# Performance work log

Measured on AMD Instinct MI355X. Metric: run time of the kernel, lower is better.

Reference implementation:

```python
import jax, jax.numpy as jnp
import numpy as np

KERNEL_SIZE = 2
DILATION = 2


def aconv(x, A, shift):
    # x: [n, c, v, l], A: [v, w]; temporal roll + zero-mask first `shift` steps,
    # then node diffusion x . A over the node axis.
    xr = jnp.roll(x, shift, axis=3)
    if shift > 0:
        xr = xr.at[..., :shift].set(0.0)
    return jnp.einsum('ncvl,vw->ncwl', xr, A)


def setup_inputs() -> dict:
    key = jax.random.key(0)
    ks = jax.random.split(key, 7)
    N, C, V, L, E, CO = 32, 64, 500, 64, 10, 64
    return {
        'x': jax.random.normal(ks[0], (N, C, V, L), dtype=jnp.float32),
        'nodevec1': jax.random.normal(ks[1], (V, E), dtype=jnp.float32),
        'nodevec2': jax.random.normal(ks[2], (E, V), dtype=jnp.float32),
        'et_w': jax.random.normal(ks[3], (E, E), dtype=jnp.float32),
        'et_b': jax.random.normal(ks[4], (E,), dtype=jnp.float32),
        'mlp_w': jax.random.normal(ks[5], (CO, (1 + KERNEL_SIZE) * C), dtype=jnp.float32) * 0.05,
        'mlp_b': jax.random.normal(ks[6], (CO,), dtype=jnp.float32),
    }


def reference(x, nodevec1, nodevec2, et_w, et_b, mlp_w, mlp_b):
    out = [x]
    x2 = x
    shift = 0
    # hop 0: adaptive adjacency from node embeddings
    adp = jax.nn.softmax(jax.nn.relu(nodevec1 @ nodevec2), axis=1)
    x1 = aconv(x2, adp, shift)
    out.append(x1)
    shift = DILATION
    x2 = x1
    for i in range(KERNEL_SIZE - 1):
        # emb_trans: affine update of both node embeddings
        nodevec1 = nodevec1 @ et_w + et_b
        nodevec2 = (nodevec2.T @ et_w + et_b).T
        adp = jax.nn.softmax(jax.nn.relu(nodevec1 @ nodevec2), axis=1)
        x1 = aconv(x2, adp, shift)
        out.append(x1)
        shift = shift + DILATION
        x2 = x1
    h = jnp.concatenate(out, axis=1)  # [n, (1+K)*c, v, l]
    # 1x1 conv == channel matmul; dropout is identity at inference
    h = jnp.einsum('ncvl,oc->novl', h, mlp_w) + mlp_b[None, :, None, None]
    return h
```

## Files before the change

### kernel.cpp

```cpp
#include <hip/hip_runtime.h>
#include <hip/hip_bf16.h>

#define NB 32
#define CC 64
#define VV 500
#define LL 64
#define EE 10
#define CO 64
#define DIL 2
#define VP 512
#define SL (VV * LL)

typedef unsigned short u16;
typedef unsigned int   u32;
typedef __attribute__((ext_vector_type(8))) short bf16x8;
typedef __attribute__((ext_vector_type(4))) float f32x4;

__device__ __forceinline__ float bf2f(u16 u) {
    union { u32 i; float f; } c; c.i = ((u32)u) << 16; return c.f;
}
__device__ __forceinline__ u16 f2bf(float f) {
    union { float f; u32 i; } c; c.f = f;
    u32 x = c.i;
    u32 r = (x + 0x7fffu + ((x >> 16) & 1u)) >> 16;
    return (u16)r;
}

__global__ void emb_kernel(const float* __restrict__ nv1, const float* __restrict__ nv2,
                           const float* __restrict__ et_w, const float* __restrict__ et_b,
                           const float* __restrict__ mlp_w,
                           float* __restrict__ nv1t, float* __restrict__ nv2t,
                           u16* __restrict__ wb) {
    int idx = blockIdx.x * blockDim.x + threadIdx.x;
    if (idx < VV * EE) {
        int v = idx / EE, e = idx - v * EE;
        float s = et_b[e];
        #pragma unroll
        for (int f = 0; f < EE; f++) s += nv1[v * EE + f] * et_w[f * EE + e];
        nv1t[idx] = s;
    } else if (idx < 2 * VV * EE) {
        int k = idx - VV * EE;
        int e = k / VV, v = k - e * VV;
        float s = et_b[e];
        #pragma unroll
        for (int f = 0; f < EE; f++) s += nv2[f * VV + v] * et_w[f * EE + e];
        nv2t[k] = s;
    } else if (idx < 2 * VV * EE + CO * 3 * CC) {
        int k = idx - 2 * VV * EE;
        wb[k] = f2bf(mlp_w[k]);
    }
}

__global__ __launch_bounds__(64) void adj2_kernel(const float* __restrict__ nv1,
                                                  const float* __restrict__ nv2,
                                                  const float* __restrict__ nv1t,
                                                  const float* __restrict__ nv2t,
                                                  u16* __restrict__ Atb0,
                                                  u16* __restrict__ Atb1) {
    const int which = blockIdx.x >> 9;
    const int v = blockIdx.x & (VP - 1);
    const float* p1 = which ? nv1t : nv1;
    const float* p2 = which ? nv2t : nv2;
    u16* Atb = which ? Atb1 : Atb0;
    const int lane = threadIdx.x;
    if (v >= VV) {
        #pragma unroll
        for (int j = 0; j < 8; j++) Atb[(size_t)(lane + 64 * j) * VP + v] = 0;
        return;
    }
    float e1[EE];
    #pragma unroll
    for (int e = 0; e < EE; e++) e1[e] = p1[v * EE + e];

    float r[8];
    float m = -1e30f;
    #pragma unroll
    for (int j = 0; j < 8; j++) {
        int w = lane + 64 * j;
        if (w < VV) {
            float s = 0.f;
            #pragma unroll
            for (int e = 0; e < EE; e++) s += e1[e] * p2[e * VV + w];
            r[j] = fmaxf(s, 0.f);
            m = fmaxf(m, r[j]);
        } else {
            r[j] = -1e30f;
        }
    }
    #pragma unroll
    for (int off = 32; off > 0; off >>= 1) m = fmaxf(m, __shfl_xor(m, off));

    float p[8];
    float sum = 0.f;
    #pragma unroll
    for (int j = 0; j < 8; j++) {
        int w = lane + 64 * j;
        if (w < VV) { p[j] = expf(r[j] - m); sum += p[j]; }
    }
    #pragma unroll
    for (int off = 32; off > 0; off >>= 1) sum += __shfl_xor(sum, off);
    float inv = 1.f / sum;
    #pragma unroll
    for (int j = 0; j < 8; j++) {
        int w = lane + 64 * j;
        Atb[(size_t)w * VP + v] = (w < VV) ? f2bf(p[j] * inv) : (u16)0;
    }
}

__global__ __launch_bounds__(512, 2) void hops_fused(const float* __restrict__ x,
                                                     const u16* __restrict__ Atb0,
                                                     const u16* __restrict__ Atb1,
                                                     u16* __restrict__ x1g,
                                                     u16* __restrict__ x2g) {
    __shared__ u16 Xt[2][LL * VP];
    const int bid = blockIdx.x;
    const int tid = threadIdx.x;
    const int lane = tid & 63;
    const int wv = tid >> 6;
    const int wr = wv * 64;
    const size_t base0 = (size_t)(2 * bid) * (VV * LL);
    const size_t base1 = base0 + (VV * LL);

    {
        const int lquad = lane & 15;
        const int vsub = lane >> 4;
        const int l0 = 4 * lquad;
        #pragma unroll
        for (int pl = 0; pl < 2; ++pl) {
            char* ldsb = (char*)Xt[pl];
            const float* xp = x + (pl ? base1 : base0);
            #pragma unroll
            for (int i = 0; i < 8; ++i) {
                const int vp = wv * 32 + i * 4 + vsub;
                const int v0 = 2 * vp;
                u32 pk0, pk1, pk2, pk3;
                if (v0 < VV) {
                    const float* xa = xp + v0 * LL + l0;
                    float4 fa = *(const float4*)xa;
                    float4 fb = *(const float4*)(xa + LL);
                    pk0 = (u32)f2bf(fa.x) | ((u32)f2bf(fb.x) << 16);
                    pk1 = (u32)f2bf(fa.y) | ((u32)f2bf(fb.y) << 16);
                    pk2 = (u32)f2bf(fa.z) | ((u32)f2bf(fb.z) << 16);
                    pk3 = (u32)f2bf(fa.w) | ((u32)f2bf(fb.w) << 16);
                } else {
                    pk0 = pk1 = pk2 = pk3 = 0;
                }
                const int vb = 4 * vp;
                int l = l0;
                *(u32*)(ldsb + l * (VP * 2) + (vb ^ ((l & 7) << 4))) = pk0; l++;
                *(u32*)(ldsb + l * (VP * 2) + (vb ^ ((l & 7) << 4))) = pk1; l++;
                *(u32*)(ldsb + l * (VP * 2) + (vb ^ ((l & 7) << 4))) = pk2; l++;
                *(u32*)(ldsb + l * (VP * 2) + (vb ^ ((l & 7) << 4))) = pk3;
            }
        }
    }
    __syncthreads();

    const int r15 = lane & 15;
    const int kg = lane >> 4;
    const char* lds0 = (const char*)Xt[0];
    const char* lds1 = (const char*)Xt[1];
    int lrow[4], lswz[4];
    #pragma unroll
    for (int ct = 0; ct < 4; ct++) {
        const int l = ct * 16 + r15;
        lrow[ct] = l * (VP * 2);
        lswz[ct] = (l & 7) << 4;
    }
    const u16* arow0[4];
    const u16* arow1[4];
    #pragma unroll
    for (int rt = 0; rt < 4; rt++) {
        const size_t ro = (size_t)(wr + rt * 16 + r15) * VP + kg * 8;
        arow0[rt] = Atb0 + ro;
        arow1[rt] = Atb1 + ro;
    }

    f32x4 acc0[4][4], acc1[4][4];
    #pragma unroll
    for (int rt = 0; rt < 4; rt++)
        #pragma unroll
        for (int ct = 0; ct < 4; ct++) {
            acc0[rt][ct] = (f32x4){0.f, 0.f, 0.f, 0.f};
            acc1[rt][ct] = (f32x4){0.f, 0.f, 0.f, 0.f};
        }

    #pragma unroll
    for (int kb = 0; kb < VP; kb += 32) {
        bf16x8 a[4], b0[4], b1[4];
        #pragma unroll
        for (int rt = 0; rt < 4; rt++)
            a[rt] = *(const bf16x8*)(arow0[rt] + kb);
        #pragma unroll
        for (int ct = 0; ct < 4; ct++) {
            const int ko = (kb * 2 + kg * 16) ^ lswz[ct];
            b0[ct] = *(const bf16x8*)(lds0 + lrow[ct] + ko);
            b1[ct] = *(const bf16x8*)(lds1 + lrow[ct] + ko);
        }
        __builtin_amdgcn_s_setprio(1);
        #pragma unroll
        for (int rt = 0; rt < 4; rt++)
            #pragma unroll
            for (int ct = 0; ct < 4; ct++) {
                acc0[rt][ct] = __builtin_amdgcn_mfma_f32_16x16x32_bf16(a[rt], b0[ct], acc0[rt][ct], 0, 0, 0);
                acc1[rt][ct] = __builtin_amdgcn_mfma_f32_16x16x32_bf16(a[rt], b1[ct], acc1[rt][ct], 0, 0, 0);
            }
        __builtin_amdgcn_s_setprio(0);
    }

    #pragma unroll
    for (int pl = 0; pl < 2; ++pl) {
        u16* xo = x1g + (pl ? base1 : base0);
        #pragma unroll
        for (int rt = 0; rt < 4; rt++) {
            #pragma unroll
            for (int ct = 0; ct < 4; ct++) {
                const int col = ct * 16 + r15;
                const int wbase = wr + rt * 16 + kg * 4;
                f32x4 c = pl ? acc1[rt][ct] : acc0[rt][ct];
                #pragma unroll
                for (int r = 0; r < 4; r++) {
                    int w = wbase + r;
                    if (w < VV) xo[w * LL + col] = f2bf(c[r]);
                }
            }
        }
    }
    __syncthreads();

    {
        #pragma unroll
        for (int pl = 0; pl < 2; ++pl) {
            char* ldsw = (char*)Xt[pl];
            {
                const int l = tid >> 8;
                const int j = tid & 255;
                *(u32*)(ldsw + l * (VP * 2) + 4 * j) = 0;
            }
            #pragma unroll
            for (int rt = 0; rt < 4; rt++) {
                const int wb2 = (wr + rt * 16 + kg * 4) * 2;
                #pragma unroll
                for (int ct = 0; ct < 4; ct++) {
                    const int col = ct * 16 + r15;
                    const int ln = col + DIL;
                    if (ln < LL) {
                        f32x4 c = pl ? acc1[rt][ct] : acc0[rt][ct];
                        u32 plo = (u32)f2bf(c[0]) | ((u32)f2bf(c[1]) << 16);
                        u32 phi = (u32)f2bf(c[2]) | ((u32)f2bf(c[3]) << 16);
                        const int swz = (ln & 7) << 4;
                        char* p = ldsw + ln * (VP * 2);
                        *(u32*)(p + (wb2 ^ swz)) = plo;
                        *(u32*)(p + ((wb2 + 4) ^ swz)) = phi;
                    }
                }
            }
        }
    }
    __syncthreads();

    #pragma unroll
    for (int rt = 0; rt < 4; rt++)
        #pragma unroll
        for (int ct = 0; ct < 4; ct++) {
            acc0[rt][ct] = (f32x4){0.f, 0.f, 0.f, 0.f};
            acc1[rt][ct] = (f32x4){0.f, 0.f, 0.f, 0.f};
        }

    #pragma unroll
    for (int kb = 0; kb < VP; kb += 32) {
        bf16x8 a[4], b0[4], b1[4];
        #pragma unroll
        for (int rt = 0; rt < 4; rt++)
            a[rt] = *(const bf16x8*)(arow1[rt] + kb);
        #pragma unroll
        for (int ct = 0; ct < 4; ct++) {
            const int ko = (kb * 2 + kg * 16) ^ lswz[ct];
            b0[ct] = *(const bf16x8*)(lds0 + lrow[ct] + ko);
            b1[ct] = *(const bf16x8*)(lds1 + lrow[ct] + ko);
        }
        __builtin_amdgcn_s_setprio(1);
        #pragma unroll
        for (int rt = 0; rt < 4; rt++)
            #pragma unroll
            for (int ct = 0; ct < 4; ct++) {
                acc0[rt][ct] = __builtin_amdgcn_mfma_f32_16x16x32_bf16(a[rt], b0[ct], acc0[rt][ct], 0, 0, 0);
                acc1[rt][ct] = __builtin_amdgcn_mfma_f32_16x16x32_bf16(a[rt], b1[ct], acc1[rt][ct], 0, 0, 0);
            }
        __builtin_amdgcn_s_setprio(0);
    }

    #pragma unroll
    for (int pl = 0; pl < 2; ++pl) {
        u16* xo = x2g + (pl ? base1 : base0);
        #pragma unroll
        for (int rt = 0; rt < 4; rt++) {
            #pragma unroll
            for (int ct = 0; ct < 4; ct++) {
                const int col = ct * 16 + r15;
                const int wbase = wr + rt * 16 + kg * 4;
                f32x4 c = pl ? acc1[rt][ct] : acc0[rt][ct];
                #pragma unroll
                for (int r = 0; r < 4; r++) {
                    int w = wbase + r;
                    if (w < VV) xo[w * LL + col] = f2bf(c[r]);
                }
            }
        }
    }
}

__global__ __launch_bounds__(256, 3) void mlp_mfma(const float* __restrict__ x,
                                                   const u16* __restrict__ x1,
                                                   const u16* __restrict__ x2,
                                                   const u16* __restrict__ wb,
                                                   const float* __restrict__ b,
                                                   float* __restrict__ out) {
    __shared__ u16 Ht[128 * 192];
    const int bid = blockIdx.x;
    const int n = bid / (SL / 128);
    const int st = bid - n * (SL / 128);
    const int s0 = st * 128;
    const int tid = threadIdx.x;

    const int lane = tid & 63;
    const int wv = tid >> 6;
    const int obase = (wv & 1) * 32;
    const int sbase = (wv >> 1) * 64;
    const int r15 = lane & 15;
    const int kg = lane >> 4;

    bf16x8 afrag[2][6];
    #pragma unroll
    for (int rt = 0; rt < 2; rt++)
        #pragma unroll
        for (int ks = 0; ks < 6; ks++)
            afrag[rt][ks] = *(const bf16x8*)(wb + (obase + rt * 16 + r15) * (3 * CC) + ks * 32 + kg * 8);

    {
        char* ldsb = (char*)Ht;
        const int squad = tid >> 3;
        const int pgroup = tid & 7;
        const int sq0 = 4 * squad;
        #pragma unroll
        for (int i = 0; i < 12; ++i) {
            const int P = i * 8 + pgroup;
            const int c = 2 * P;
            u32 pk0, pk1, pk2, pk3;
            if (i < 4) {
                const float* fsrc = x + ((size_t)n * CC + c) * SL + s0 + sq0;
                float4 va = *(const float4*)fsrc;
                float4 vb = *(const float4*)(fsrc + SL);
                pk0 = (u32)f2bf(va.x) | ((u32)f2bf(vb.x) << 16);
                pk1 = (u32)f2bf(va.y) | ((u32)f2bf(vb.y) << 16);
                pk2 = (u32)f2bf(va.z) | ((u32)f2bf(vb.z) << 16);
                pk3 = (u32)f2bf(va.w) | ((u32)f2bf(vb.w) << 16);
            } else {
                const u16* bsrc = (i < 8)
                    ? x1 + ((size_t)n * CC + (c - CC)) * SL + s0 + sq0
                    : x2 + ((size_t)n * CC + (c - 2 * CC)) * SL + s0 + sq0;
                uint2 va = *(const uint2*)bsrc;
                uint2 vb = *(const uint2*)(bsrc + SL);
                pk0 = (va.x & 0xffffu) | (vb.x << 16);
                pk1 = (va.x >> 16) | (vb.x & 0xffff0000u);
                pk2 = (va.y & 0xffffu) | (vb.y << 16);
                pk3 = (va.y >> 16) | (vb.y & 0xffff0000u);
            }
            int s = sq0;
            *(u32*)(ldsb + s * 384 + ((4 * P) ^ ((s & 7) << 4))) = pk0; s++;
            *(u32*)(ldsb + s * 384 + ((4 * P) ^ ((s & 7) << 4))) = pk1; s++;
            *(u32*)(ldsb + s * 384 + ((4 * P) ^ ((s & 7) << 4))) = pk2; s++;
            *(u32*)(ldsb + s * 384 + ((4 * P) ^ ((s & 7) << 4))) = pk3;
        }
    }
    __syncthreads();

    f32x4 acc[2][4];
    #pragma unroll
    for (int rt = 0; rt < 2; rt++)
        #pragma unroll
        for (int ct = 0; ct < 4; ct++)
            acc[rt][ct] = (f32x4){0.f, 0.f, 0.f, 0.f};

    const char* ldsb = (const char*)Ht;
    #pragma unroll
    for (int ks = 0; ks < 6; ks++) {
        bf16x8 bfr[4];
        #pragma unroll
        for (int ct = 0; ct < 4; ct++) {
            const int s = sbase + ct * 16 + r15;
            bfr[ct] = *(const bf16x8*)(ldsb + s * 384 + ((ks * 64 + kg * 16) ^ ((s & 7) << 4)));
        }
        #pragma unroll
        for (int rt = 0; rt < 2; rt++)
            #pragma unroll
            for (int ct = 0; ct < 4; ct++)
                acc[rt][ct] = __builtin_amdgcn_mfma_f32_16x16x32_bf16(afrag[rt][ks], bfr[ct], acc[rt][ct], 0, 0, 0);
    }

    #pragma unroll
    for (int rt = 0; rt < 2; rt++) {
        #pragma unroll
        for (int r = 0; r < 4; r++) {
            const int o = obase + rt * 16 + kg * 4 + r;
            const float bias = b[o];
            float* orow = out + ((size_t)n * CO + o) * SL + s0 + sbase;
            #pragma unroll
            for (int ct = 0; ct < 4; ct++)
                orow[ct * 16 + r15] = acc[rt][ct][r] + bias;
        }
    }
}

extern "C" void kernel_launch(void* const* d_in, const int* in_sizes, int n_in,
                              void* d_out, int out_size, void* d_ws, size_t ws_size,
                              hipStream_t stream) {
    const float* x     = (const float*)d_in[0];
    const float* nv1   = (const float*)d_in[1];
    const float* nv2   = (const float*)d_in[2];
    const float* et_w  = (const float*)d_in[3];
    const float* et_b  = (const float*)d_in[4];
    const float* mlp_w = (const float*)d_in[5];
    const float* mlp_b = (const float*)d_in[6];
    float* out = (float*)d_out;

    char* wsb = (char*)d_ws;
    size_t off = 0;
    auto alloc = [&](size_t bytes) {
        size_t o = off;
        off += (bytes + 255) & ~(size_t)255;
        return o;
    };
    u16*   Atb0 = (u16*)(wsb + alloc((size_t)VP * VP * 2));
    u16*   Atb1 = (u16*)(wsb + alloc((size_t)VP * VP * 2));
    float* nv1t = (float*)(wsb + alloc((size_t)VV * EE * 4));
    float* nv2t = (float*)(wsb + alloc((size_t)EE * VV * 4));
    u16*   wb   = (u16*)(wsb + alloc((size_t)CO * 3 * CC * 2));
    u16*   x1   = (u16*)(wsb + alloc((size_t)NB * CC * VV * LL * 2));
    u16*   x2   = (u16*)(wsb + alloc((size_t)NB * CC * VV * LL * 2));
    (void)in_sizes; (void)n_in; (void)out_size; (void)ws_size;

    const int embN = 2 * VV * EE + CO * 3 * CC;
    emb_kernel<<<(embN + 255) / 256, 256, 0, stream>>>(nv1, nv2, et_w, et_b, mlp_w, nv1t, nv2t, wb);
    adj2_kernel<<<2 * VP, 64, 0, stream>>>(nv1, nv2, nv1t, nv2t, Atb0, Atb1);
    hops_fused<<<NB * CC / 2, 512, 0, stream>>>(x, Atb0, Atb1, x1, x2);
    mlp_mfma<<<NB * (SL / 128), 256, 0, stream>>>(x, x1, x2, wb, mlp_b, out);
}
```

Measured before the change: 445.7 us.

## Pipeline plane-1 staging behind plane-0 MFMA and process planes sequentially

The hop kernel now processes the two batch planes one after another with a single accumulator set instead of two interleaved sets. The global load and bf16 conversion of the second plane's input into LDS is software-pipelined inside the first plane's MFMA loop, hiding that load latency behind compute. Write-backs and the shifted LDS rewrites are interleaved between per-plane GEMMs. Halving the accumulators reduces register pressure, at the cost of less MFMA independence per k-step and extra barriers.

```diff
diff --git a/kernel.cpp b/kernel.cpp
--- a/kernel.cpp
+++ b/kernel.cpp
@@ -121,45 +121,12 @@
     const size_t base0 = (size_t)(2 * bid) * (VV * LL);
     const size_t base1 = base0 + (VV * LL);
 
-    {
-        const int lquad = lane & 15;
-        const int vsub = lane >> 4;
-        const int l0 = 4 * lquad;
-        #pragma unroll
-        for (int pl = 0; pl < 2; ++pl) {
-            char* ldsb = (char*)Xt[pl];
-            const float* xp = x + (pl ? base1 : base0);
-            #pragma unroll
-            for (int i = 0; i < 8; ++i) {
-                const int vp = wv * 32 + i * 4 + vsub;
-                const int v0 = 2 * vp;
-                u32 pk0, pk1, pk2, pk3;
-                if (v0 < VV) {
-                    const float* xa = xp + v0 * LL + l0;
-                    float4 fa = *(const float4*)xa;
-                    float4 fb = *(const float4*)(xa + LL);
-                    pk0 = (u32)f2bf(fa.x) | ((u32)f2bf(fb.x) << 16);
-                    pk1 = (u32)f2bf(fa.y) | ((u32)f2bf(fb.y) << 16);
-                    pk2 = (u32)f2bf(fa.z) | ((u32)f2bf(fb.z) << 16);
-                    pk3 = (u32)f2bf(fa.w) | ((u32)f2bf(fb.w) << 16);
-                } else {
-                    pk0 = pk1 = pk2 = pk3 = 0;
-                }
-                const int vb = 4 * vp;
-                int l = l0;
-                *(u32*)(ldsb + l * (VP * 2) + (vb ^ ((l & 7) << 4))) = pk0; l++;
-                *(u32*)(ldsb + l * (VP * 2) + (vb ^ ((l & 7) << 4))) = pk1; l++;
-                *(u32*)(ldsb + l * (VP * 2) + (vb ^ ((l & 7) << 4))) = pk2; l++;
-                *(u32*)(ldsb + l * (VP * 2) + (vb ^ ((l & 7) << 4))) = pk3;
-            }
-        }
-    }
-    __syncthreads();
-
+    const int lquad = lane & 15;
+    const int vsub = lane >> 4;
+    const int l0 = 4 * lquad;
     const int r15 = lane & 15;
     const int kg = lane >> 4;
-    const char* lds0 = (const char*)Xt[0];
-    const char* lds1 = (const char*)Xt[1];
+
     int lrow[4], lswz[4];
     #pragma unroll
     for (int ct = 0; ct < 4; ct++) {
@@ -176,48 +143,39 @@
         arow1[rt] = Atb1 + ro;
     }
 
-    f32x4 acc0[4][4], acc1[4][4];
-    #pragma unroll
-    for (int rt = 0; rt < 4; rt++)
-        #pragma unroll
-        for (int ct = 0; ct < 4; ct++) {
-            acc0[rt][ct] = (f32x4){0.f, 0.f, 0.f, 0.f};
-            acc1[rt][ct] = (f32x4){0.f, 0.f, 0.f, 0.f};
-        }
-
-    #pragma unroll
-    for (int kb = 0; kb < VP; kb += 32) {
-        bf16x8 a[4], b0[4], b1[4];
+    f32x4 acc[4][4];
+
+    auto zacc = [&]() {
         #pragma unroll
         for (int rt = 0; rt < 4; rt++)
-            a[rt] = *(const bf16x8*)(arow0[rt] + kb);
-        #pragma unroll
-        for (int ct = 0; ct < 4; ct++) {
-            const int ko = (kb * 2 + kg * 16) ^ lswz[ct];
-            b0[ct] = *(const bf16x8*)(lds0 + lrow[ct] + ko);
-            b1[ct] = *(const bf16x8*)(lds1 + lrow[ct] + ko);
-        }
+            #pragma unroll
+            for (int ct = 0; ct < 4; ct++)
+                acc[rt][ct] = (f32x4){0.f, 0.f, 0.f, 0.f};
+    };
+    auto kstep = [&](const u16* const arow[4], const char* ldsX, int s) {
+        bf16x8 a[4], b[4];
+        #pragma unroll
+        for (int rt = 0; rt < 4; rt++)
+            a[rt] = *(const bf16x8*)(arow[rt] + s * 32);
+        #pragma unroll
+        for (int ct = 0; ct < 4; ct++)
+            b[ct] = *(const bf16x8*)(ldsX + lrow[ct] + ((s * 64 + kg * 16) ^ lswz[ct]));
         __builtin_amdgcn_s_setprio(1);
         #pragma unroll
         for (int rt = 0; rt < 4; rt++)
             #pragma unroll
-            for (int ct = 0; ct < 4; ct++) {
-                acc0[rt][ct] = __builtin_amdgcn_mfma_f32_16x16x32_bf16(a[rt], b0[ct], acc0[rt][ct], 0, 0, 0);
-                acc1[rt][ct] = __builtin_amdgcn_mfma_f32_16x16x32_bf16(a[rt], b1[ct], acc1[rt][ct], 0, 0, 0);
-            }
+            for (int ct = 0; ct < 4; ct++)
+                acc[rt][ct] = __builtin_amdgcn_mfma_f32_16x16x32_bf16(a[rt], b[ct], acc[rt][ct], 0, 0, 0);
         __builtin_amdgcn_s_setprio(0);
-    }
-
-    #pragma unroll
-    for (int pl = 0; pl < 2; ++pl) {
-        u16* xo = x1g + (pl ? base1 : base0);
+    };
+    auto store_plane = [&](u16* xo) {
         #pragma unroll
         for (int rt = 0; rt < 4; rt++) {
             #pragma unroll
             for (int ct = 0; ct < 4; ct++) {
                 const int col = ct * 16 + r15;
                 const int wbase = wr + rt * 16 + kg * 4;
-                f32x4 c = pl ? acc1[rt][ct] : acc0[rt][ct];
+                f32x4 c = acc[rt][ct];
                 #pragma unroll
                 for (int r = 0; r < 4; r++) {
                     int w = wbase + r;
@@ -225,89 +183,128 @@
                 }
             }
         }
-    }
-    __syncthreads();
-
-    {
-        #pragma unroll
-        for (int pl = 0; pl < 2; ++pl) {
-            char* ldsw = (char*)Xt[pl];
-            {
-                const int l = tid >> 8;
-                const int j = tid & 255;
-                *(u32*)(ldsw + l * (VP * 2) + 4 * j) = 0;
-            }
-            #pragma unroll
-            for (int rt = 0; rt < 4; rt++) {
-                const int wb2 = (wr + rt * 16 + kg * 4) * 2;
-                #pragma unroll
-                for (int ct = 0; ct < 4; ct++) {
-                    const int col = ct * 16 + r15;
-                    const int ln = col + DIL;
-                    if (ln < LL) {
-                        f32x4 c = pl ? acc1[rt][ct] : acc0[rt][ct];
-                        u32 plo = (u32)f2bf(c[0]) | ((u32)f2bf(c[1]) << 16);
-                        u32 phi = (u32)f2bf(c[2]) | ((u32)f2bf(c[3]) << 16);
-                        const int swz = (ln & 7) << 4;
-                        char* p = ldsw + ln * (VP * 2);
-                        *(u32*)(p + (wb2 ^ swz)) = plo;
-                        *(u32*)(p + ((wb2 + 4) ^ swz)) = phi;
-                    }
+    };
+    auto rewrite = [&](char* ldsw) {
+        {
+            const int l = tid >> 8;
+            const int j = tid & 255;
+            *(u32*)(ldsw + l * (VP * 2) + 4 * j) = 0;
+        }
+        #pragma unroll
+        for (int rt = 0; rt < 4; rt++) {
+            const int wb2 = (wr + rt * 16 + kg * 4) * 2;
+            #pragma unroll
+            for (int ct = 0; ct < 4; ct++) {
+                const int col = ct * 16 + r15;
+                const int ln = col + DIL;
+                if (ln < LL) {
+                    f32x4 c = acc[rt][ct];
+                    u32 plo = (u32)f2bf(c[0]) | ((u32)f2bf(c[1]) << 16);
+                    u32 phi = (u32)f2bf(c[2]) | ((u32)f2bf(c[3]) << 16);
+                    const int swz = (ln & 7) << 4;
+                    char* p = ldsw + ln * (VP * 2);
+                    *(u32*)(p + (wb2 ^ swz)) = plo;
+                    *(u32*)(p + ((wb2 + 4) ^ swz)) = phi;
                 }
             }
         }
-    }
+    };
+    auto sload = [&](int i, float4& A, float4& B) {
+        const int v0 = 2 * (wv * 32 + i * 4 + vsub);
+        if (v0 < VV) {
+            const float* xa = x + base1 + v0 * LL + l0;
+            A = *(const float4*)xa;
+            B = *(const float4*)(xa + LL);
+        }
+    };
+    auto swrite = [&](int i, float4 A, float4 B) {
+        const int vp = wv * 32 + i * 4 + vsub;
+        const int v0 = 2 * vp;
+        u32 pk0, pk1, pk2, pk3;
+        if (v0 < VV) {
+            pk0 = (u32)f2bf(A.x) | ((u32)f2bf(B.x) << 16);
+            pk1 = (u32)f2bf(A.y) | ((u32)f2bf(B.y) << 16);
+            pk2 = (u32)f2bf(A.z) | ((u32)f2bf(B.z) << 16);
+            pk3 = (u32)f2bf(A.w) | ((u32)f2bf(B.w) << 16);
+        } else {
+            pk0 = pk1 = pk2 = pk3 = 0;
+        }
+        char* ldsb = (char*)Xt[1];
+        const int vb = 4 * vp;
+        int l = l0;
+        *(u32*)(ldsb + l * (VP * 2) + (vb ^ ((l & 7) << 4))) = pk0; l++;
+        *(u32*)(ldsb + l * (VP * 2) + (vb ^ ((l & 7) << 4))) = pk1; l++;
+        *(u32*)(ldsb + l * (VP * 2) + (vb ^ ((l & 7) << 4))) = pk2; l++;
+        *(u32*)(ldsb + l * (VP * 2) + (vb ^ ((l & 7) << 4))) = pk3;
+    };
+
+    {
+        char* ldsb = (char*)Xt[0];
+        #pragma unroll
+        for (int i = 0; i < 8; ++i) {
+            const int vp = wv * 32 + i * 4 + vsub;
+            const int v0 = 2 * vp;
+            u32 pk0, pk1, pk2, pk3;
+            if (v0 < VV) {
+                const float* xa = x + base0 + v0 * LL + l0;
+                float4 fa = *(const float4*)xa;
+                float4 fb = *(const float4*)(xa + LL);
+                pk0 = (u32)f2bf(fa.x) | ((u32)f2bf(fb.x) << 16);
+                pk1 = (u32)f2bf(fa.y) | ((u32)f2bf(fb.y) << 16);
+                pk2 = (u32)f2bf(fa.z) | ((u32)f2bf(fb.z) << 16);
+                pk3 = (u32)f2bf(fa.w) | ((u32)f2bf(fb.w) << 16);
+            } else {
+                pk0 = pk1 = pk2 = pk3 = 0;
+            }
+            const int vb = 4 * vp;
+            int l = l0;
+            *(u32*)(ldsb + l * (VP * 2) + (vb ^ ((l & 7) << 4))) = pk0; l++;
+            *(u32*)(ldsb + l * (VP * 2) + (vb ^ ((l & 7) << 4))) = pk1; l++;
+            *(u32*)(ldsb + l * (VP * 2) + (vb ^ ((l & 7) << 4))) = pk2; l++;
+            *(u32*)(ldsb + l * (VP * 2) + (vb ^ ((l & 7) << 4))) = pk3;
+        }
+    }
+    float4 fa, fb, fa2, fb2;
+    sload(0, fa, fb);
     __syncthreads();
 
-    #pragma unroll
-    for (int rt = 0; rt < 4; rt++)
-        #pragma unroll
-        for (int ct = 0; ct < 4; ct++) {
-            acc0[rt][ct] = (f32x4){0.f, 0.f, 0.f, 0.f};
-            acc1[rt][ct] = (f32x4){0.f, 0.f, 0.f, 0.f};
-        }
-
-    #pragma unroll
-    for (int kb = 0; kb < VP; kb += 32) {
-        bf16x8 a[4], b0[4], b1[4];
-        #pragma unroll
-        for (int rt = 0; rt < 4; rt++)
-            a[rt] = *(const bf16x8*)(arow1[rt] + kb);
-        #pragma unroll
-        for (int ct = 0; ct < 4; ct++) {
-            const int ko = (kb * 2 + kg * 16) ^ lswz[ct];
-            b0[ct] = *(const bf16x8*)(lds0 + lrow[ct] + ko);
-            b1[ct] = *(const bf16x8*)(lds1 + lrow[ct] + ko);
-        }
-        __builtin_amdgcn_s_setprio(1);
-        #pragma unroll
-        for (int rt = 0; rt < 4; rt++)
-            #pragma unroll
-            for (int ct = 0; ct < 4; ct++) {
-                acc0[rt][ct] = __builtin_amdgcn_mfma_f32_16x16x32_bf16(a[rt], b0[ct], acc0[rt][ct], 0, 0, 0);
-                acc1[rt][ct] = __builtin_amdgcn_mfma_f32_16x16x32_bf16(a[rt], b1[ct], acc1[rt][ct], 0, 0, 0);
-            }
-        __builtin_amdgcn_s_setprio(0);
-    }
-
-    #pragma unroll
-    for (int pl = 0; pl < 2; ++pl) {
-        u16* xo = x2g + (pl ? base1 : base0);
-        #pragma unroll
-        for (int rt = 0; rt < 4; rt++) {
-            #pragma unroll
-            for (int ct = 0; ct < 4; ct++) {
-                const int col = ct * 16 + r15;
-                const int wbase = wr + rt * 16 + kg * 4;
-                f32x4 c = pl ? acc1[rt][ct] : acc0[rt][ct];
-                #pragma unroll
-                for (int r = 0; r < 4; r++) {
-                    int w = wbase + r;
-                    if (w < VV) xo[w * LL + col] = f2bf(c[r]);
-                }
-            }
-        }
-    }
+    const char* lds0 = (const char*)Xt[0];
+    const char* lds1 = (const char*)Xt[1];
+
+    zacc();
+    #pragma unroll
+    for (int i = 0; i < 8; ++i) {
+        if (i + 1 < 8) sload(i + 1, fa2, fb2);
+        kstep(arow0, lds0, 2 * i);
+        swrite(i, fa, fb);
+        kstep(arow0, lds0, 2 * i + 1);
+        fa = fa2; fb = fb2;
+    }
+    __syncthreads();
+
+    store_plane(x1g + base0);
+    rewrite((char*)Xt[0]);
+
+    zacc();
+    #pragma unroll
+    for (int s = 0; s < 16; ++s) kstep(arow0, lds1, s);
+    __syncthreads();
+
+    store_plane(x1g + base1);
+    rewrite((char*)Xt[1]);
+
+    zacc();
+    #pragma unroll
+    for (int s = 0; s < 16; ++s) kstep(arow1, lds0, s);
+    __syncthreads();
+
+    store_plane(x2g + base0);
+
+    zacc();
+    #pragma unroll
+    for (int s = 0; s < 16; ++s) kstep(arow1, lds1, s);
+
+    store_plane(x2g + base1);
 }
 
 __global__ __launch_bounds__(256, 3) void mlp_mfma(const float* __restrict__ x,
```

Result: slower. 524.1 us (+17.6%).
